# Kernel optimization log

Hardware: AMD Instinct MI355X
Metric: run time of the kernel (lower is better)

Reference implementation:

```python
import jax, jax.numpy as jnp
import numpy as np

N_NODES = 50000
N_EDGES = 800000
N_GRAPHS = 256
D = 256
L = 3
BN_EPS = 1e-5


def setup_inputs() -> dict:
    key = jax.random.key(0)
    ks = jax.random.split(key, 8)
    x = jax.random.normal(ks[0], (N_NODES, D), dtype=jnp.float32)
    edge_index = jax.random.randint(ks[1], (2, N_EDGES), 0, N_NODES, dtype=jnp.int64)
    batch = jnp.sort(jax.random.randint(ks[2], (N_NODES,), 0, N_GRAPHS, dtype=jnp.int64))
    # small init scale keeps ReLU/BN chain numerically tame
    w1 = jax.random.normal(ks[3], (L, D, D), dtype=jnp.float32) * 0.05
    b1 = jnp.zeros((L, D), dtype=jnp.float32)
    w2 = jax.random.normal(ks[4], (L, D, D), dtype=jnp.float32) * 0.05
    b2 = jnp.zeros((L, D), dtype=jnp.float32)
    gamma = jnp.ones((L, D), dtype=jnp.float32)
    beta = jnp.zeros((L, D), dtype=jnp.float32)
    return {"x": x, "edge_index": edge_index, "batch": batch,
            "w1": w1, "b1": b1, "w2": w2, "b2": b2,
            "gamma": gamma, "beta": beta}


def reference(x, edge_index, batch, w1, b1, w2, b2, gamma, beta):
    src = edge_index[0]  # message senders (x_j)
    dst = edge_index[1]  # aggregation targets (x_i)
    h = x
    xs = []
    for i in range(L):
        # GINConv (eps=0): MLP(x_i + sum_{j in N(i)} x_j)
        agg = jax.ops.segment_sum(h[src], dst, num_segments=N_NODES)  # [N, D]
        z = h + agg
        z = jnp.maximum(z @ w1[i] + b1[i], 0.0) @ w2[i] + b2[i]  # Linear-ReLU-Linear
        z = jnp.maximum(z, 0.0)  # F.relu after conv
        # BatchNorm1d (training mode: biased batch stats over nodes)
        mean = jnp.mean(z, axis=0)
        var = jnp.var(z, axis=0)
        z = (z - mean) * jax.lax.rsqrt(var + BN_EPS) * gamma[i] + beta[i]
        xs.append(z)
        h = z
    # global_add_pool per layer, then concat along features -> [G, L*D]
    pooled = [jax.ops.segment_sum(xi, batch, num_segments=N_GRAPHS) for xi in xs]
    return jnp.concatenate(pooled, axis=1)
```

## Files before the change

### kernel.cpp

```cpp
#include <hip/hip_runtime.h>

#define NN 50000
#define NE 800000
#define NG 256
#define DD 256
#define NL 3
#define BN_EPS 1e-5f
#define MPAD 50048
#define CAP 96
#define MB2 782
#define NBIN 196

typedef short bf16x8 __attribute__((ext_vector_type(8)));
typedef float f32x4 __attribute__((ext_vector_type(4)));
typedef unsigned short ushort8 __attribute__((ext_vector_type(8)));

__device__ __forceinline__ unsigned short f2bf(float f) {
    unsigned int u = __float_as_uint(f);
    u += 0x7FFFu + ((u >> 16) & 1u);
    return (unsigned short)(u >> 16);
}
__device__ __forceinline__ float bf2f(unsigned short s) {
    return __uint_as_float(((unsigned int)s) << 16);
}

#define R0 3200000
#define R1 393216
#define R2 12288
#define R3 256
#define R4 256
#define R5 NBIN
#define RTOT (R0 + R1 + R2 + R3 + R4 + R5)

__global__ void k_setup(const float* __restrict__ x, const float* __restrict__ w1,
                        const float* __restrict__ w2, const int* __restrict__ batch,
                        unsigned short* __restrict__ hbf, unsigned short* __restrict__ wt,
                        unsigned short* __restrict__ zbf, int* __restrict__ gstart,
                        int* __restrict__ bin_cnt) {
    int i = blockIdx.x * blockDim.x + threadIdx.x;
    if (i < R0) {
        float4 v = ((const float4*)x)[i];
        ushort4 o;
        o.x = f2bf(v.x); o.y = f2bf(v.y); o.z = f2bf(v.z); o.w = f2bf(v.w);
        ((ushort4*)hbf)[i] = o;
        return;
    }
    i -= R0;
    if (i < R1) {
        int mat = i >> 16;
        int n = (i >> 8) & 255;
        int k = i & 255;
        const float* src = (mat < 3) ? (w1 + ((size_t)mat << 16)) : (w2 + ((size_t)(mat - 3) << 16));
        wt[i] = f2bf(src[k * 256 + n]);
        return;
    }
    i -= R1;
    if (i < R2) { zbf[NN * DD + i] = 0; return; }
    i -= R2;
    if (i < R3) { hbf[(size_t)NN * DD + i] = 0; return; }
    i -= R3;
    if (i < R4) {
        int g = i;
        int lo = 0, hi = NN;
        while (lo < hi) {
            int mid = (lo + hi) >> 1;
            if (batch[mid] < g) lo = mid + 1; else hi = mid;
        }
        gstart[g] = lo;
        if (g == 0) gstart[NG] = NN;
        return;
    }
    i -= R4;
    if (i < R5) bin_cnt[i] = 0;
}

__global__ __launch_bounds__(256) void k_bin1(const int* __restrict__ ei,
                                              int* __restrict__ bin_cnt) {
    __shared__ int hist[NBIN];
    int t = threadIdx.x;
    for (int i = t; i < NBIN; i += 256) hist[i] = 0;
    __syncthreads();
    #pragma unroll
    for (int j = 0; j < 4; ++j) {
        int e = blockIdx.x * 1024 + j * 256 + t;
        if (e < NE) atomicAdd(&hist[ei[NE + e] >> 8], 1);
    }
    __syncthreads();
    for (int i = t; i < NBIN; i += 256)
        if (hist[i]) atomicAdd(&bin_cnt[i], hist[i]);
}

__global__ void k_binscan(const int* __restrict__ bin_cnt, int* __restrict__ bin_start,
                          int* __restrict__ bin_cursor) {
    __shared__ int s[256];
    int t = threadIdx.x;
    int v = (t < NBIN) ? bin_cnt[t] : 0;
    s[t] = v;
    __syncthreads();
    #pragma unroll
    for (int d = 1; d < 256; d <<= 1) {
        int a = (t >= d) ? s[t - d] : 0;
        __syncthreads();
        s[t] += a;
        __syncthreads();
    }
    int excl = s[t] - v;
    if (t < NBIN) { bin_start[t] = excl; bin_cursor[t] = excl; }
    if (t == 0) bin_start[NBIN] = NE;
}

__global__ __launch_bounds__(256) void k_bin2(const int* __restrict__ ei,
                                              int* __restrict__ bin_cursor,
                                              unsigned int* __restrict__ binbuf) {
    __shared__ int hist[NBIN], base[NBIN], lcur[NBIN];
    int t = threadIdx.x;
    for (int i = t; i < NBIN; i += 256) { hist[i] = 0; lcur[i] = 0; }
    __syncthreads();
    int d[4], s[4];
    #pragma unroll
    for (int j = 0; j < 4; ++j) {
        int e = blockIdx.x * 1024 + j * 256 + t;
        if (e < NE) {
            s[j] = ei[e];
            d[j] = ei[NE + e];
            atomicAdd(&hist[d[j] >> 8], 1);
        } else d[j] = -1;
    }
    __syncthreads();
    for (int i = t; i < NBIN; i += 256)
        base[i] = hist[i] ? atomicAdd(&bin_cursor[i], hist[i]) : 0;
    __syncthreads();
    #pragma unroll
    for (int j = 0; j < 4; ++j) {
        if (d[j] >= 0) {
            int b = d[j] >> 8;
            int o = atomicAdd(&lcur[b], 1);
            binbuf[base[b] + o] = (unsigned)s[j] | ((unsigned)(d[j] & 255) << 16);
        }
    }
}

__global__ __launch_bounds__(256) void k_bin3(const unsigned int* __restrict__ binbuf,
                                              const int* __restrict__ bin_start,
                                              unsigned short* __restrict__ elist,
                                              int* __restrict__ deg) {
    __shared__ int ldeg[256];
    int b = blockIdx.x, t = threadIdx.x;
    ldeg[t] = 0;
    __syncthreads();
    int lo = bin_start[b], hi = bin_start[b + 1];
    for (int i = lo + t; i < hi; i += 256) {
        unsigned v = binbuf[i];
        int src = v & 0xFFFF;
        int dl = v >> 16;
        int pos = atomicAdd(&ldeg[dl], 1);
        elist[(size_t)(b * 256 + dl) * CAP + pos] = (unsigned short)src;
    }
    __syncthreads();
    int node = b * 256 + t;
    if (node < NN) deg[node] = ldeg[t];
}

__global__ __launch_bounds__(256) void k_agg_bf(const unsigned short* __restrict__ h,
                                                const int* __restrict__ deg,
                                                const unsigned short* __restrict__ elist,
                                                unsigned short* __restrict__ z0) {
    int wave = threadIdx.x >> 6;
    int lane = threadIdx.x & 63;
    int node = blockIdx.x * 4 + wave;
    int chunk = lane & 31;
    int half = lane >> 5;
    const ushort8* h8 = (const ushort8*)h;

    float acc[8];
    if (half == 0) {
        ushort8 own = h8[(size_t)node * 32 + chunk];
        #pragma unroll
        for (int j = 0; j < 8; ++j) acc[j] = bf2f(own[j]);
    } else {
        #pragma unroll
        for (int j = 0; j < 8; ++j) acc[j] = 0.f;
    }

    int n = deg[node];
    const unsigned short* el = elist + (size_t)node * CAP;
    int i = 0;
    for (; i + 8 <= n; i += 8) {
        ushort8 sv = *(const ushort8*)(el + i);
        int i0 = half ? sv[1] : sv[0];
        int i1 = half ? sv[3] : sv[2];
        int i2 = half ? sv[5] : sv[4];
        int i3 = half ? sv[7] : sv[6];
        ushort8 r0 = h8[(size_t)i0 * 32 + chunk];
        ushort8 r1 = h8[(size_t)i1 * 32 + chunk];
        ushort8 r2 = h8[(size_t)i2 * 32 + chunk];
        ushort8 r3 = h8[(size_t)i3 * 32 + chunk];
        #pragma unroll
        for (int j = 0; j < 8; ++j) acc[j] += bf2f(r0[j]);
        #pragma unroll
        for (int j = 0; j < 8; ++j) acc[j] += bf2f(r1[j]);
        #pragma unroll
        for (int j = 0; j < 8; ++j) acc[j] += bf2f(r2[j]);
        #pragma unroll
        for (int j = 0; j < 8; ++j) acc[j] += bf2f(r3[j]);
    }
    for (; i < n; i += 2) {
        int s0 = el[i];
        int s1 = (i + 1 < n) ? (int)el[i + 1] : NN;
        int idx = half ? s1 : s0;
        ushort8 r = h8[(size_t)idx * 32 + chunk];
        #pragma unroll
        for (int j = 0; j < 8; ++j) acc[j] += bf2f(r[j]);
    }

    ushort8 o;
    #pragma unroll
    for (int j = 0; j < 8; ++j) {
        float other = __shfl_xor(acc[j], 32);
        o[j] = f2bf(acc[j] + other);
    }
    if (half == 0) ((ushort8*)z0)[(size_t)node * 32 + chunk] = o;
}

__global__ __launch_bounds__(256, 2) void k_mlp(const unsigned short* __restrict__ A,
                                                const unsigned short* __restrict__ BT1,
                                                const unsigned short* __restrict__ BT2,
                                                const float* __restrict__ b1,
                                                const float* __restrict__ b2,
                                                float* __restrict__ Cout,
                                                float* __restrict__ pstat) {
    __shared__ short As[64 * 64];
    __shared__ short Bs[256 * 64];
    __shared__ short H1[64 * 256];
    __shared__ float spart[256][2];
    int tid = threadIdx.x;
    int lane = tid & 63;
    int wc = tid >> 6;
    long m0 = (long)blockIdx.x * 64;
    const int r = lane & 15, hi = lane >> 4;

    f32x4 acc[4][4];
    #pragma unroll
    for (int m = 0; m < 4; ++m)
        #pragma unroll
        for (int n = 0; n < 4; ++n)
            acc[m][n] = (f32x4){0.f, 0.f, 0.f, 0.f};

    for (int k0 = 0; k0 < DD; k0 += 64) {
        #pragma unroll
        for (int p = 0; p < 2; ++p) {
            int flat = p * 256 + tid;
            int row = flat >> 3, c8 = flat & 7;
            int slot = c8 ^ (row & 7);
            *(bf16x8*)(As + row * 64 + slot * 8) =
                *(const bf16x8*)(A + (m0 + row) * DD + k0 + c8 * 8);
        }
        #pragma unroll
        for (int p = 0; p < 8; ++p) {
            int flat = p * 256 + tid;
            int row = flat >> 3, c8 = flat & 7;
            int slot = c8 ^ (row & 7);
            *(bf16x8*)(Bs + row * 64 + slot * 8) =
                *(const bf16x8*)(BT1 + (long)row * DD + k0 + c8 * 8);
        }
        __syncthreads();
        bf16x8 af[4][2], bfr[4][2];
        #pragma unroll
        for (int m = 0; m < 4; ++m) {
            int row = m * 16 + r;
            #pragma unroll
            for (int kk = 0; kk < 2; ++kk) {
                int slot = (kk * 4 + hi) ^ (row & 7);
                af[m][kk] = *(const bf16x8*)(As + row * 64 + slot * 8);
            }
        }
        #pragma unroll
        for (int n = 0; n < 4; ++n) {
            int col = wc * 64 + n * 16 + r;
            #pragma unroll
            for (int kk = 0; kk < 2; ++kk) {
                int slot = (kk * 4 + hi) ^ (col & 7);
                bfr[n][kk] = *(const bf16x8*)(Bs + col * 64 + slot * 8);
            }
        }
        #pragma unroll
        for (int kk = 0; kk < 2; ++kk)
            #pragma unroll
            for (int m = 0; m < 4; ++m)
                #pragma unroll
                for (int n = 0; n < 4; ++n)
                    acc[m][n] = __builtin_amdgcn_mfma_f32_16x16x32_bf16(af[m][kk], bfr[n][kk], acc[m][n], 0, 0, 0);
        __syncthreads();
    }

    #pragma unroll
    for (int n = 0; n < 4; ++n) {
        int col = wc * 64 + n * 16 + r;
        float bv = b1[col];
        int g = col >> 3, j8 = col & 7;
        #pragma unroll
        for (int m = 0; m < 4; ++m) {
            #pragma unroll
            for (int j = 0; j < 4; ++j) {
                int row = m * 16 + hi * 4 + j;
                float v = acc[m][n][j] + bv;
                v = v > 0.f ? v : 0.f;
                H1[row * 256 + (g ^ (row & 7)) * 8 + j8] = (short)f2bf(v);
            }
        }
    }
    #pragma unroll
    for (int m = 0; m < 4; ++m)
        #pragma unroll
        for (int n = 0; n < 4; ++n)
            acc[m][n] = (f32x4){0.f, 0.f, 0.f, 0.f};
    __syncthreads();

    for (int k0 = 0; k0 < DD; k0 += 64) {
        #pragma unroll
        for (int p = 0; p < 8; ++p) {
            int flat = p * 256 + tid;
            int row = flat >> 3, c8 = flat & 7;
            int slot = c8 ^ (row & 7);
            *(bf16x8*)(Bs + row * 64 + slot * 8) =
                *(const bf16x8*)(BT2 + (long)row * DD + k0 + c8 * 8);
        }
        __syncthreads();
        bf16x8 af[4][2], bfr[4][2];
        #pragma unroll
        for (int m = 0; m < 4; ++m) {
            int row = m * 16 + r;
            #pragma unroll
            for (int kk = 0; kk < 2; ++kk) {
                int g = (k0 >> 3) + kk * 4 + hi;
                af[m][kk] = *(const bf16x8*)(H1 + row * 256 + (g ^ (row & 7)) * 8);
            }
        }
        #pragma unroll
        for (int n = 0; n < 4; ++n) {
            int col = wc * 64 + n * 16 + r;
            #pragma unroll
            for (int kk = 0; kk < 2; ++kk) {
                int slot = (kk * 4 + hi) ^ (col & 7);
                bfr[n][kk] = *(const bf16x8*)(Bs + col * 64 + slot * 8);
            }
        }
        #pragma unroll
        for (int kk = 0; kk < 2; ++kk)
            #pragma unroll
            for (int m = 0; m < 4; ++m)
                #pragma unroll
                for (int n = 0; n < 4; ++n)
                    acc[m][n] = __builtin_amdgcn_mfma_f32_16x16x32_bf16(af[m][kk], bfr[n][kk], acc[m][n], 0, 0, 0);
        __syncthreads();
    }

    #pragma unroll
    for (int n = 0; n < 4; ++n) {
        int col = wc * 64 + n * 16 + r;
        float bv = b2[col];
        float cs = 0.f, cs2 = 0.f;
        #pragma unroll
        for (int m = 0; m < 4; ++m) {
            #pragma unroll
            for (int j = 0; j < 4; ++j) {
                long grow = m0 + m * 16 + hi * 4 + j;
                float v = acc[m][n][j] + bv;
                v = v > 0.f ? v : 0.f;
                Cout[grow * DD + col] = v;
                float vm = (grow < NN) ? v : 0.f;
                cs += vm; cs2 += vm * vm;
            }
        }
        cs  += __shfl_xor(cs, 16);  cs  += __shfl_xor(cs, 32);
        cs2 += __shfl_xor(cs2, 16); cs2 += __shfl_xor(cs2, 32);
        if (hi == 0) {
            spart[col][0] = cs;
            spart[col][1] = cs2;
        }
    }
    __syncthreads();
    pstat[(size_t)blockIdx.x * 512 + tid] = spart[tid][0];
    pstat[(size_t)blockIdx.x * 512 + 256 + tid] = spart[tid][1];
}

__global__ __launch_bounds__(256) void k_bnscale2(const float* __restrict__ pstat,
                                                  const float* __restrict__ gamma,
                                                  const float* __restrict__ beta,
                                                  float* __restrict__ ss) {
    int c = blockIdx.x;
    int t = threadIdx.x;
    float s = 0.f, s2 = 0.f;
    for (int mb = t; mb < MB2; mb += 256) {
        s  += pstat[(size_t)mb * 512 + c];
        s2 += pstat[(size_t)mb * 512 + 256 + c];
    }
    __shared__ float rs[256], rs2[256];
    rs[t] = s; rs2[t] = s2;
    __syncthreads();
    #pragma unroll
    for (int d = 128; d > 0; d >>= 1) {
        if (t < d) { rs[t] += rs[t + d]; rs2[t] += rs2[t + d]; }
        __syncthreads();
    }
    if (t == 0) {
        float mean = rs[0] * (1.0f / NN);
        float var = rs2[0] * (1.0f / NN) - mean * mean;
        float sc = gamma[c] * rsqrtf(var + BN_EPS);
        ss[c] = sc;
        ss[DD + c] = beta[c] - mean * sc;
    }
}

template<int LAST>
__global__ __launch_bounds__(512) void k_bnpool(const float* __restrict__ z,
                                                const float* __restrict__ ss,
                                                const int* __restrict__ gstart,
                                                unsigned short* __restrict__ hbf,
                                                float* __restrict__ out, int layer) {
    __shared__ float4 red[16][32];
    int g = blockIdx.x;
    int ch = blockIdx.y;
    int t = threadIdx.x;
    int q = t & 31, rg = t >> 5;
    int cq = ch * 32 + q;
    float4 sc = ((const float4*)ss)[cq];
    float4 sh = ((const float4*)(ss + DD))[cq];
    int lo = gstart[g], hi = gstart[g + 1];
    float4 s = {0.f, 0.f, 0.f, 0.f};
    const float4* z4 = (const float4*)z;
    ushort4* h4 = (ushort4*)hbf;
    for (int r = lo + rg; r < hi; r += 16) {
        float4 v = z4[(size_t)r * 64 + cq];
        v.x = v.x * sc.x + sh.x;
        v.y = v.y * sc.y + sh.y;
        v.z = v.z * sc.z + sh.z;
        v.w = v.w * sc.w + sh.w;
        s.x += v.x; s.y += v.y; s.z += v.z; s.w += v.w;
        if (!LAST) {
            ushort4 o;
            o.x = f2bf(v.x); o.y = f2bf(v.y); o.z = f2bf(v.z); o.w = f2bf(v.w);
            h4[(size_t)r * 64 + cq] = o;
        }
    }
    red[rg][q] = s;
    __syncthreads();
    #pragma unroll
    for (int d = 8; d > 0; d >>= 1) {
        if (rg < d) {
            float4 a = red[rg][q], b = red[rg + d][q];
            a.x += b.x; a.y += b.y; a.z += b.z; a.w += b.w;
            red[rg][q] = a;
        }
        __syncthreads();
    }
    if (rg == 0) {
        ((float4*)(out + (size_t)g * (NL * DD) + layer * DD))[cq] = red[0][q];
    }
}

extern "C" void kernel_launch(void* const* d_in, const int* in_sizes, int n_in,
                              void* d_out, int out_size, void* d_ws, size_t ws_size,
                              hipStream_t stream) {
    const float* x     = (const float*)d_in[0];
    const int*   ei    = (const int*)d_in[1];
    const int*   batch = (const int*)d_in[2];
    const float* w1    = (const float*)d_in[3];
    const float* b1    = (const float*)d_in[4];
    const float* w2    = (const float*)d_in[5];
    const float* b2    = (const float*)d_in[6];
    const float* gamma = (const float*)d_in[7];
    const float* beta  = (const float*)d_in[8];
    float* out = (float*)d_out;

    char* ws = (char*)d_ws;
    size_t off = 0;
    auto alloc = [&](size_t bytes) -> void* {
        void* p = ws + off;
        off += (bytes + 255) & ~size_t(255);
        return p;
    };
    float*          buf0 = (float*)alloc((size_t)MPAD * DD * 4);
    unsigned short* zbf  = (unsigned short*)alloc((size_t)MPAD * DD * 2);
    unsigned short* hbf  = (unsigned short*)alloc((size_t)(NN + 64) * DD * 2);
    unsigned short* wt   = (unsigned short*)alloc((size_t)6 * DD * DD * 2);
    int* deg    = (int*)alloc((size_t)NN * 4);
    unsigned short* elist = (unsigned short*)alloc((size_t)NN * CAP * 2);
    unsigned int* binbuf = (unsigned int*)alloc((size_t)NE * 4);
    int* bin_cnt    = (int*)alloc(NBIN * 4);
    int* bin_start  = (int*)alloc((NBIN + 1) * 4);
    int* bin_cursor = (int*)alloc(NBIN * 4);
    int* gstart = (int*)alloc((size_t)(NG + 1) * 4);
    float* pstat = (float*)alloc((size_t)MB2 * 512 * 4);
    float* ss   = (float*)alloc(2 * DD * 4);

    k_setup<<<(RTOT + 255) / 256, 256, 0, stream>>>(x, w1, w2, batch, hbf, wt, zbf, gstart, bin_cnt);
    const int EB = (NE + 1023) / 1024;
    k_bin1<<<EB, 256, 0, stream>>>(ei, bin_cnt);
    k_binscan<<<1, 256, 0, stream>>>(bin_cnt, bin_start, bin_cursor);
    k_bin2<<<EB, 256, 0, stream>>>(ei, bin_cursor, binbuf);
    k_bin3<<<NBIN, 256, 0, stream>>>(binbuf, bin_start, elist, deg);

    for (int l = 0; l < NL; ++l) {
        k_agg_bf<<<NN / 4, 256, 0, stream>>>(hbf, deg, elist, zbf);
        k_mlp<<<MB2, 256, 0, stream>>>(zbf, wt + (size_t)l * DD * DD,
                                       wt + (size_t)(3 + l) * DD * DD,
                                       b1 + l * DD, b2 + l * DD, buf0, pstat);
        k_bnscale2<<<DD, 256, 0, stream>>>(pstat, gamma + l * DD, beta + l * DD, ss);
        if (l < NL - 1)
            k_bnpool<0><<<dim3(NG, 2), 512, 0, stream>>>(buf0, ss, gstart, hbf, out, l);
        else
            k_bnpool<1><<<dim3(NG, 2), 512, 0, stream>>>(buf0, ss, gstart, hbf, out, l);
    }
}
```

Baseline: 393.3 us.

## Store MLP output as bf16 and bin edges into fixed-capacity buckets

```diff
diff --git a/kernel.cpp b/kernel.cpp
--- a/kernel.cpp
+++ b/kernel.cpp
@@ -10,6 +10,7 @@
 #define CAP 96
 #define MB2 782
 #define NBIN 196
+#define BINCAP 4608
 
 typedef short bf16x8 __attribute__((ext_vector_type(8)));
 typedef float f32x4 __attribute__((ext_vector_type(4)));
@@ -74,43 +75,8 @@
     if (i < R5) bin_cnt[i] = 0;
 }
 
-__global__ __launch_bounds__(256) void k_bin1(const int* __restrict__ ei,
-                                              int* __restrict__ bin_cnt) {
-    __shared__ int hist[NBIN];
-    int t = threadIdx.x;
-    for (int i = t; i < NBIN; i += 256) hist[i] = 0;
-    __syncthreads();
-    #pragma unroll
-    for (int j = 0; j < 4; ++j) {
-        int e = blockIdx.x * 1024 + j * 256 + t;
-        if (e < NE) atomicAdd(&hist[ei[NE + e] >> 8], 1);
-    }
-    __syncthreads();
-    for (int i = t; i < NBIN; i += 256)
-        if (hist[i]) atomicAdd(&bin_cnt[i], hist[i]);
-}
-
-__global__ void k_binscan(const int* __restrict__ bin_cnt, int* __restrict__ bin_start,
-                          int* __restrict__ bin_cursor) {
-    __shared__ int s[256];
-    int t = threadIdx.x;
-    int v = (t < NBIN) ? bin_cnt[t] : 0;
-    s[t] = v;
-    __syncthreads();
-    #pragma unroll
-    for (int d = 1; d < 256; d <<= 1) {
-        int a = (t >= d) ? s[t - d] : 0;
-        __syncthreads();
-        s[t] += a;
-        __syncthreads();
-    }
-    int excl = s[t] - v;
-    if (t < NBIN) { bin_start[t] = excl; bin_cursor[t] = excl; }
-    if (t == 0) bin_start[NBIN] = NE;
-}
-
 __global__ __launch_bounds__(256) void k_bin2(const int* __restrict__ ei,
-                                              int* __restrict__ bin_cursor,
+                                              int* __restrict__ bin_cnt,
                                               unsigned int* __restrict__ binbuf) {
     __shared__ int hist[NBIN], base[NBIN], lcur[NBIN];
     int t = threadIdx.x;
@@ -128,29 +94,30 @@
     }
     __syncthreads();
     for (int i = t; i < NBIN; i += 256)
-        base[i] = hist[i] ? atomicAdd(&bin_cursor[i], hist[i]) : 0;
+        base[i] = hist[i] ? atomicAdd(&bin_cnt[i], hist[i]) : 0;
     __syncthreads();
     #pragma unroll
     for (int j = 0; j < 4; ++j) {
         if (d[j] >= 0) {
             int b = d[j] >> 8;
             int o = atomicAdd(&lcur[b], 1);
-            binbuf[base[b] + o] = (unsigned)s[j] | ((unsigned)(d[j] & 255) << 16);
+            binbuf[(size_t)b * BINCAP + base[b] + o] = (unsigned)s[j] | ((unsigned)(d[j] & 255) << 16);
         }
     }
 }
 
 __global__ __launch_bounds__(256) void k_bin3(const unsigned int* __restrict__ binbuf,
-                                              const int* __restrict__ bin_start,
+                                              const int* __restrict__ bin_cnt,
                                               unsigned short* __restrict__ elist,
                                               int* __restrict__ deg) {
     __shared__ int ldeg[256];
     int b = blockIdx.x, t = threadIdx.x;
     ldeg[t] = 0;
     __syncthreads();
-    int lo = bin_start[b], hi = bin_start[b + 1];
-    for (int i = lo + t; i < hi; i += 256) {
-        unsigned v = binbuf[i];
+    int cnt = bin_cnt[b];
+    const unsigned int* bb = binbuf + (size_t)b * BINCAP;
+    for (int i = t; i < cnt; i += 256) {
+        unsigned v = bb[i];
         int src = v & 0xFFFF;
         int dl = v >> 16;
         int pos = atomicAdd(&ldeg[dl], 1);
@@ -227,7 +194,7 @@
                                                 const unsigned short* __restrict__ BT2,
                                                 const float* __restrict__ b1,
                                                 const float* __restrict__ b2,
-                                                float* __restrict__ Cout,
+                                                unsigned short* __restrict__ Cout,
                                                 float* __restrict__ pstat) {
     __shared__ short As[64 * 64];
     __shared__ short Bs[256 * 64];
@@ -367,7 +334,7 @@
                 long grow = m0 + m * 16 + hi * 4 + j;
                 float v = acc[m][n][j] + bv;
                 v = v > 0.f ? v : 0.f;
-                Cout[grow * DD + col] = v;
+                Cout[grow * DD + col] = f2bf(v);
                 float vm = (grow < NN) ? v : 0.f;
                 cs += vm; cs2 += vm * vm;
             }
@@ -413,7 +380,7 @@
 }
 
 template<int LAST>
-__global__ __launch_bounds__(512) void k_bnpool(const float* __restrict__ z,
+__global__ __launch_bounds__(512) void k_bnpool(const unsigned short* __restrict__ z,
                                                 const float* __restrict__ ss,
                                                 const int* __restrict__ gstart,
                                                 unsigned short* __restrict__ hbf,
@@ -428,14 +395,15 @@
     float4 sh = ((const float4*)(ss + DD))[cq];
     int lo = gstart[g], hi = gstart[g + 1];
     float4 s = {0.f, 0.f, 0.f, 0.f};
-    const float4* z4 = (const float4*)z;
+    const ushort4* z4 = (const ushort4*)z;
     ushort4* h4 = (ushort4*)hbf;
     for (int r = lo + rg; r < hi; r += 16) {
-        float4 v = z4[(size_t)r * 64 + cq];
-        v.x = v.x * sc.x + sh.x;
-        v.y = v.y * sc.y + sh.y;
-        v.z = v.z * sc.z + sh.z;
-        v.w = v.w * sc.w + sh.w;
+        ushort4 zv = z4[(size_t)r * 64 + cq];
+        float4 v;
+        v.x = bf2f(zv.x) * sc.x + sh.x;
+        v.y = bf2f(zv.y) * sc.y + sh.y;
+        v.z = bf2f(zv.z) * sc.z + sh.z;
+        v.w = bf2f(zv.w) * sc.w + sh.w;
         s.x += v.x; s.y += v.y; s.z += v.z; s.w += v.w;
         if (!LAST) {
             ushort4 o;
@@ -480,36 +448,32 @@
         off += (bytes + 255) & ~size_t(255);
         return p;
     };
-    float*          buf0 = (float*)alloc((size_t)MPAD * DD * 4);
+    unsigned short* zB   = (unsigned short*)alloc((size_t)MPAD * DD * 2);
     unsigned short* zbf  = (unsigned short*)alloc((size_t)MPAD * DD * 2);
     unsigned short* hbf  = (unsigned short*)alloc((size_t)(NN + 64) * DD * 2);
     unsigned short* wt   = (unsigned short*)alloc((size_t)6 * DD * DD * 2);
     int* deg    = (int*)alloc((size_t)NN * 4);
     unsigned short* elist = (unsigned short*)alloc((size_t)NN * CAP * 2);
-    unsigned int* binbuf = (unsigned int*)alloc((size_t)NE * 4);
+    unsigned int* binbuf = (unsigned int*)alloc((size_t)NBIN * BINCAP * 4);
     int* bin_cnt    = (int*)alloc(NBIN * 4);
-    int* bin_start  = (int*)alloc((NBIN + 1) * 4);
-    int* bin_cursor = (int*)alloc(NBIN * 4);
     int* gstart = (int*)alloc((size_t)(NG + 1) * 4);
     float* pstat = (float*)alloc((size_t)MB2 * 512 * 4);
     float* ss   = (float*)alloc(2 * DD * 4);
 
     k_setup<<<(RTOT + 255) / 256, 256, 0, stream>>>(x, w1, w2, batch, hbf, wt, zbf, gstart, bin_cnt);
     const int EB = (NE + 1023) / 1024;
-    k_bin1<<<EB, 256, 0, stream>>>(ei, bin_cnt);
-    k_binscan<<<1, 256, 0, stream>>>(bin_cnt, bin_start, bin_cursor);
-    k_bin2<<<EB, 256, 0, stream>>>(ei, bin_cursor, binbuf);
-    k_bin3<<<NBIN, 256, 0, stream>>>(binbuf, bin_start, elist, deg);
+    k_bin2<<<EB, 256, 0, stream>>>(ei, bin_cnt, binbuf);
+    k_bin3<<<NBIN, 256, 0, stream>>>(binbuf, bin_cnt, elist, deg);
 
     for (int l = 0; l < NL; ++l) {
         k_agg_bf<<<NN / 4, 256, 0, stream>>>(hbf, deg, elist, zbf);
         k_mlp<<<MB2, 256, 0, stream>>>(zbf, wt + (size_t)l * DD * DD,
                                        wt + (size_t)(3 + l) * DD * DD,
-                                       b1 + l * DD, b2 + l * DD, buf0, pstat);
+                                       b1 + l * DD, b2 + l * DD, zB, pstat);
         k_bnscale2<<<DD, 256, 0, stream>>>(pstat, gamma + l * DD, beta + l * DD, ss);
         if (l < NL - 1)
-            k_bnpool<0><<<dim3(NG, 2), 512, 0, stream>>>(buf0, ss, gstart, hbf, out, l);
+            k_bnpool<0><<<dim3(NG, 2), 512, 0, stream>>>(zB, ss, gstart, hbf, out, l);
         else
-            k_bnpool<1><<<dim3(NG, 2), 512, 0, stream>>>(buf0, ss, gstart, hbf, out, l);
-    }
-}
+            k_bnpool<1><<<dim3(NG, 2), 512, 0, stream>>>(zB, ss, gstart, hbf, out, l);
+    }
+}
```

Result: faster. 361.4 us (median of 2 runs) (-8.1%).
